# Performance work log

Hardware: AMD Instinct MI355X
Metric: run time of the kernel (lower is better)

The kernel has to match this reference:

```python
import jax, jax.numpy as jnp
import numpy as np

D_MODEL = 1024
NHEAD = 16
D_HEAD = D_MODEL // NHEAD


def setup_inputs() -> dict:
    key = jax.random.key(0)
    ks = jax.random.split(key, 11)
    B, S = 4, 1024
    s = 1.0 / np.sqrt(D_MODEL)
    inp = {
        'q_in': jax.random.normal(ks[0], (B, S, D_MODEL), jnp.float32),
        'k_in': jax.random.normal(ks[1], (B, S, D_MODEL), jnp.float32),
        'v_in': jax.random.normal(ks[2], (B, S, D_MODEL), jnp.float32),
        'Wq': jax.random.normal(ks[3], (D_MODEL, D_MODEL), jnp.float32) * s,
        'bq': jnp.zeros((D_MODEL,), jnp.float32),
        'Wk': jax.random.normal(ks[4], (D_MODEL, D_MODEL), jnp.float32) * s,
        'bk': jnp.zeros((D_MODEL,), jnp.float32),
        'Wv': jax.random.normal(ks[5], (D_MODEL, D_MODEL), jnp.float32) * s,
        'bv': jnp.zeros((D_MODEL,), jnp.float32),
        'Wo': jax.random.normal(ks[6], (D_MODEL, D_MODEL), jnp.float32) * s,
        'bo': jnp.zeros((D_MODEL,), jnp.float32),
    }
    return inp


def reference(q_in, k_in, v_in, Wq, bq, Wk, bk, Wv, bv, Wo, bo):
    B, Sq, _ = q_in.shape
    Sk = k_in.shape[1]
    # Linear projections (torch Linear: x @ W.T + b; here W stored as [in, out])
    Q = q_in @ Wq + bq
    K = k_in @ Wk + bk
    V = v_in @ Wv + bv
    # [B, H, S, Dh]
    Qh = Q.reshape(B, Sq, NHEAD, D_HEAD).transpose(0, 2, 1, 3)
    Kh = K.reshape(B, Sk, NHEAD, D_HEAD).transpose(0, 2, 1, 3)
    Vh = V.reshape(B, Sk, NHEAD, D_HEAD).transpose(0, 2, 1, 3)
    scores = jnp.einsum('bhqd,bhkd->bhqk', Qh, Kh) / jnp.sqrt(jnp.float32(D_HEAD))
    attn_weights = jax.nn.softmax(scores, axis=-1)
    attn = jnp.einsum('bhqk,bhkd->bhqd', attn_weights, Vh)
    attn = attn.transpose(0, 2, 1, 3).reshape(B, Sq, D_MODEL)
    out = attn @ Wo + bo
    return out
```

## Files before the change

kernel.cpp:

```cpp
#include <hip/hip_runtime.h>
#include <hip/hip_bf16.h>
#include <cstdint>
#include <cstddef>

typedef __bf16 bf16_t;
typedef __bf16 bf16x8 __attribute__((ext_vector_type(8)));
typedef __bf16 bf16x4 __attribute__((ext_vector_type(4)));
typedef float f32x4 __attribute__((ext_vector_type(4)));

#define DM 1024
#define NHEAD 16
#define DHEAD 64

#define QSCALE 0.18033688011112042f
#define PSHIFT 4.0f
#define RS 72

#define WAITVM(N) asm volatile("s_waitcnt vmcnt(" #N ")" ::: "memory")

__device__ __forceinline__ void gload_lds16(const void* g, void* l) {
    __builtin_amdgcn_global_load_lds(
        (const __attribute__((address_space(1))) void*)g,
        (__attribute__((address_space(3))) void*)l,
        16, 0, 0);
}

__device__ __forceinline__ uint4 cvt8(float4 lo, float4 hi) {
    union { bf16_t b[8]; uint4 u; } o;
    o.b[0] = (bf16_t)lo.x; o.b[1] = (bf16_t)lo.y; o.b[2] = (bf16_t)lo.z; o.b[3] = (bf16_t)lo.w;
    o.b[4] = (bf16_t)hi.x; o.b[5] = (bf16_t)hi.y; o.b[6] = (bf16_t)hi.z; o.b[7] = (bf16_t)hi.w;
    return o.u;
}

__global__ void prep(
    const float* __restrict__ q_in, const float* __restrict__ k_in, const float* __restrict__ v_in,
    bf16_t* __restrict__ Xq, bf16_t* __restrict__ Xk, bf16_t* __restrict__ Xv,
    const float* __restrict__ w0, const float* __restrict__ w1,
    const float* __restrict__ w2, const float* __restrict__ w3,
    bf16_t* __restrict__ t0, bf16_t* __restrict__ t1,
    bf16_t* __restrict__ t2, bf16_t* __restrict__ t3)
{
    __shared__ float tile[64][65];
    int id = blockIdx.x;
    if (id < 6144) {
        int plane = id >> 11;
        int blk = id & 2047;
        const float* x = plane == 0 ? q_in : plane == 1 ? k_in : v_in;
        bf16_t* y      = plane == 0 ? Xq   : plane == 1 ? Xk   : Xv;
        int i = (blk * 256 + threadIdx.x) * 8;
        float4 lo = *(const float4*)&x[i];
        float4 hi = *(const float4*)&x[i + 4];
        *(uint4*)&y[i] = cvt8(lo, hi);
    } else {
        int t = id - 6144;
        int zi = t >> 8;
        int blk = t & 255;
        const float* w = zi == 0 ? w0 : zi == 1 ? w1 : zi == 2 ? w2 : w3;
        bf16_t* wt     = zi == 0 ? t0 : zi == 1 ? t1 : zi == 2 ? t2 : t3;
        int bx = (blk & 15) * 64;
        int by = (blk >> 4) * 64;
        int tx = threadIdx.x & 63, ty = threadIdx.x >> 6;
        for (int j = 0; j < 64; j += 4)
            tile[ty + j][tx] = w[(size_t)(by + ty + j) * DM + bx + tx];
        __syncthreads();
        int nl = threadIdx.x >> 3;
        int kl = (threadIdx.x & 7) * 8;
        for (int j = 0; j < 64; j += 32) {
            int n = nl + j;
            union { bf16_t b[8]; uint4 u; } o;
            for (int i = 0; i < 8; i++)
                o.b[i] = (bf16_t)tile[kl + i][n];
            *(uint4*)&wt[(size_t)(bx + n) * DM + by + kl] = o.u;
        }
    }
}

template <int MODE>
__device__ __forceinline__ void gemm_body(
    const bf16_t* __restrict__ A, const bf16_t* __restrict__ Bt,
    const float* __restrict__ bias, float scale,
    bf16_t* __restrict__ Cb,
    int r0, int c0, bf16_t* AsP, bf16_t* BsP)
{
    const int K = 1024;
    int tid  = threadIdx.x;
    int wave = tid >> 6;
    int lane = tid & 63;
    int quad = lane >> 4;
    int ln   = lane & 15;
    int wr   = wave >> 1;
    int wc   = wave & 1;

    f32x4 acc[4][4];
    for (int rb = 0; rb < 4; rb++)
        for (int cb = 0; cb < 4; cb++)
            acc[rb][cb] = (f32x4){0.f, 0.f, 0.f, 0.f};

    int sr = tid >> 2;
    int sk = (tid & 3) * 8;

    const bf16_t* gA0 = &A[(size_t)(r0 + sr) * K + sk];
    const bf16_t* gA1 = gA0 + (size_t)64 * K;
    const bf16_t* gB0 = &Bt[(size_t)(c0 + sr) * K + sk];
    const bf16_t* gB1 = gB0 + (size_t)64 * K;
    char* lA = (char*)AsP + wave * 1024;
    char* lB = (char*)BsP + wave * 1024;

    auto STAGE = [&](int s) {
        int off = (s & 3) * 8192;
        int k = s * 32;
        gload_lds16(gA0 + k, lA + off);
        gload_lds16(gA1 + k, lA + off + 4096);
        gload_lds16(gB0 + k, lB + off);
        gload_lds16(gB1 + k, lB + off + 4096);
    };
    auto COMPUTE = [&](int t) {
        const bf16_t* Ab = AsP + (t & 3) * 4096;
        const bf16_t* Bb = BsP + (t & 3) * 4096;
        bf16x8 af[4], bfv[4];
        for (int rb = 0; rb < 4; rb++)
            af[rb] = *(const bf16x8*)&Ab[(wr * 64 + rb * 16 + ln) * 32 + quad * 8];
        for (int cb = 0; cb < 4; cb++)
            bfv[cb] = *(const bf16x8*)&Bb[(wc * 64 + cb * 16 + ln) * 32 + quad * 8];
        for (int rb = 0; rb < 4; rb++)
            for (int cb = 0; cb < 4; cb++)
                acc[rb][cb] = __builtin_amdgcn_mfma_f32_16x16x32_bf16(af[rb], bfv[cb], acc[rb][cb], 0, 0, 0);
    };

    STAGE(0); STAGE(1); STAGE(2);

    for (int t = 0; t < 29; ++t) {
        WAITVM(8);
        __builtin_amdgcn_s_barrier();
        STAGE(t + 3);
        COMPUTE(t);
    }
    WAITVM(8); __builtin_amdgcn_s_barrier(); COMPUTE(29);
    WAITVM(4); __builtin_amdgcn_s_barrier(); COMPUTE(30);
    WAITVM(0); __builtin_amdgcn_s_barrier(); COMPUTE(31);

    for (int rb = 0; rb < 4; rb++) {
        for (int cb = 0; cb < 4; cb++) {
            int C = c0 + wc * 64 + cb * 16 + ln;
            for (int r = 0; r < 4; r++) {
                int R = r0 + wr * 64 + rb * 16 + quad * 4 + r;
                float v = acc[rb][cb][r];
                if (MODE == 1) {
                    int b = R >> 10, s = R & 1023;
                    int h = C >> 6,  d = C & 63;
                    Cb[(((size_t)b * NHEAD + h) * 1024 + s) * DHEAD + d] =
                        (bf16_t)((v + bias[C]) * scale);
                } else {
                    Cb[((size_t)(C >> 10) * 1024 + R) * 1024 + (C & 1023)] =
                        (bf16_t)(v + bias[R]);
                }
            }
        }
    }
}

__global__ __launch_bounds__(256) void gemm_qkv(
    const bf16_t* __restrict__ Xq, const bf16_t* __restrict__ Xk, const bf16_t* __restrict__ Xv,
    const bf16_t* __restrict__ Wtq, const bf16_t* __restrict__ Wtk, const bf16_t* __restrict__ Wtv,
    const float* __restrict__ bq, const float* __restrict__ bk, const float* __restrict__ bv,
    bf16_t* __restrict__ Qd, bf16_t* __restrict__ Kd, bf16_t* __restrict__ Vt)
{
    __shared__ __align__(16) bf16_t As[4 * 128 * 32];
    __shared__ __align__(16) bf16_t Bs[4 * 128 * 32];
    int z = blockIdx.z;
    if (z == 0) {
        gemm_body<1>(Xq, Wtq, bq, QSCALE, Qd,
                     blockIdx.x * 128, blockIdx.y * 128, As, Bs);
    } else if (z == 1) {
        gemm_body<1>(Xk, Wtk, bk, 1.0f, Kd,
                     blockIdx.x * 128, blockIdx.y * 128, As, Bs);
    } else {
        gemm_body<2>(Wtv, Xv, bv, 1.0f, Vt,
                     blockIdx.y * 128, blockIdx.x * 128, As, Bs);
    }
}

__global__ __launch_bounds__(256) void gemm_out(
    const bf16_t* __restrict__ At, const bf16_t* __restrict__ Wto,
    const float* __restrict__ bo, float* __restrict__ out)
{
    const int K = 1024;
    __shared__ __align__(16) bf16_t As[4 * 64 * 32];
    __shared__ __align__(16) bf16_t Bs[4 * 128 * 32];

    int tid  = threadIdx.x;
    int wave = tid >> 6;
    int lane = tid & 63;
    int quad = lane >> 4;
    int ln   = lane & 15;

    int r0 = blockIdx.x * 64;
    int c0 = blockIdx.y * 128;

    f32x4 acc[4][2];
    for (int rb = 0; rb < 4; rb++)
        for (int cb = 0; cb < 2; cb++)
            acc[rb][cb] = (f32x4){0.f, 0.f, 0.f, 0.f};

    int sr = tid >> 2;
    int sk = (tid & 3) * 8;

    const bf16_t* gA0 = At  + (size_t)(r0 + sr) * K + sk;
    const bf16_t* gB0 = Wto + (size_t)(c0 + sr) * K + sk;
    const bf16_t* gB1 = gB0 + (size_t)64 * K;
    char* lA = (char*)As + wave * 1024;
    char* lB = (char*)Bs + wave * 1024;

    auto STAGE = [&](int s) {
        int k = s * 32;
        gload_lds16(gA0 + k, lA + (s & 3) * 4096);
        gload_lds16(gB0 + k, lB + (s & 3) * 8192);
        gload_lds16(gB1 + k, lB + (s & 3) * 8192 + 4096);
    };
    auto COMPUTE = [&](int t) {
        const bf16_t* Ab = As + (t & 3) * 2048;
        const bf16_t* Bb = Bs + (t & 3) * 4096;
        bf16x8 af[4], bfv[2];
        for (int rb = 0; rb < 4; rb++)
            af[rb] = *(const bf16x8*)&Ab[(rb * 16 + ln) * 32 + quad * 8];
        for (int cb = 0; cb < 2; cb++)
            bfv[cb] = *(const bf16x8*)&Bb[(wave * 32 + cb * 16 + ln) * 32 + quad * 8];
        for (int rb = 0; rb < 4; rb++)
            for (int cb = 0; cb < 2; cb++)
                acc[rb][cb] = __builtin_amdgcn_mfma_f32_16x16x32_bf16(af[rb], bfv[cb], acc[rb][cb], 0, 0, 0);
    };

    STAGE(0); STAGE(1); STAGE(2);

    for (int t = 0; t < 29; ++t) {
        WAITVM(6);
        __builtin_amdgcn_s_barrier();
        STAGE(t + 3);
        COMPUTE(t);
    }
    WAITVM(6); __builtin_amdgcn_s_barrier(); COMPUTE(29);
    WAITVM(3); __builtin_amdgcn_s_barrier(); COMPUTE(30);
    WAITVM(0); __builtin_amdgcn_s_barrier(); COMPUTE(31);

    for (int rb = 0; rb < 4; rb++) {
        for (int cb = 0; cb < 2; cb++) {
            int C = c0 + wave * 32 + cb * 16 + ln;
            float bn = bo[C];
            for (int r = 0; r < 4; r++) {
                int R = r0 + rb * 16 + quad * 4 + r;
                out[(size_t)R * DM + C] = acc[rb][cb][r] + bn;
            }
        }
    }
}

__global__ __launch_bounds__(256) void attn6(
    const bf16_t* __restrict__ Q,
    const bf16_t* __restrict__ K,
    const bf16_t* __restrict__ Vt,
    bf16_t* __restrict__ O)
{
    __shared__ __align__(16) bf16_t Ks[64 * RS];
    __shared__ __align__(16) bf16_t Vs[64 * RS];
    __shared__ __align__(16) bf16_t Ps[4][32 * RS];

    int tid  = threadIdx.x;
    int wave = tid >> 6;
    int lane = tid & 63;
    int quad = lane >> 4;
    int ln   = lane & 15;

    int bh = blockIdx.x;
    int q0w = blockIdx.y * 128 + wave * 32;

    const bf16_t* Qb = Q  + (size_t)bh * 65536;
    const bf16_t* Kb = K  + (size_t)bh * 65536;
    const bf16_t* Vb = Vt + (size_t)bh * 65536;

    int srow = tid >> 3;
    int scol = (tid & 7) * 8;
    const bf16_t* gK0 = Kb + (size_t)srow * 64 + scol;
    const bf16_t* gK1 = gK0 + 32 * 64;
    const bf16_t* gV0 = Vb + (size_t)srow * 1024 + scol;
    const bf16_t* gV1 = gV0 + 32 * 1024;

    bf16x8 aq0[2], aq1[2];
    for (int h = 0; h < 2; h++) {
        aq0[h] = *(const bf16x8*)&Qb[(size_t)(q0w + h * 16 + ln) * 64 + quad * 8];
        aq1[h] = *(const bf16x8*)&Qb[(size_t)(q0w + h * 16 + ln) * 64 + 32 + quad * 8];
    }

    uint4 rK0 = *(const uint4*)gK0;
    uint4 rK1 = *(const uint4*)gK1;
    uint4 rV0 = *(const uint4*)gV0;
    uint4 rV1 = *(const uint4*)gV1;

    float l_lane[2] = {0.f, 0.f};
    f32x4 o_acc[2][4];
    for (int h = 0; h < 2; h++)
        for (int cb = 0; cb < 4; cb++)
            o_acc[h][cb] = (f32x4){0.f, 0.f, 0.f, 0.f};

    bf16_t* Pw = Ps[wave];

    for (int kt = 0; kt < 16; kt++) {
        __syncthreads();
        *(uint4*)&Ks[srow * RS + scol]        = rK0;
        *(uint4*)&Ks[(32 + srow) * RS + scol] = rK1;
        *(uint4*)&Vs[srow * RS + scol]        = rV0;
        *(uint4*)&Vs[(32 + srow) * RS + scol] = rV1;
        __syncthreads();

        if (kt < 15) {
            gK0 += 4096; gK1 += 4096; gV0 += 64; gV1 += 64;
            rK0 = *(const uint4*)gK0;
            rK1 = *(const uint4*)gK1;
            rV0 = *(const uint4*)gV0;
            rV1 = *(const uint4*)gV1;
        }

        f32x4 sc[4][2];
        for (int kb = 0; kb < 4; kb++) {
            bf16x8 kf0 = *(const bf16x8*)&Ks[(kb * 16 + ln) * RS + quad * 8];
            bf16x8 kf1 = *(const bf16x8*)&Ks[(kb * 16 + ln) * RS + 32 + quad * 8];
            for (int h = 0; h < 2; h++) {
                f32x4 a = (f32x4){0.f, 0.f, 0.f, 0.f};
                a = __builtin_amdgcn_mfma_f32_16x16x32_bf16(kf0, aq0[h], a, 0, 0, 0);
                a = __builtin_amdgcn_mfma_f32_16x16x32_bf16(kf1, aq1[h], a, 0, 0, 0);
                sc[kb][h] = a;
            }
        }

        for (int kb = 0; kb < 4; kb++) {
            for (int h = 0; h < 2; h++) {
                float p0 = __builtin_amdgcn_exp2f(sc[kb][h][0] - PSHIFT);
                float p1 = __builtin_amdgcn_exp2f(sc[kb][h][1] - PSHIFT);
                float p2 = __builtin_amdgcn_exp2f(sc[kb][h][2] - PSHIFT);
                float p3 = __builtin_amdgcn_exp2f(sc[kb][h][3] - PSHIFT);
                l_lane[h] += (p0 + p1) + (p2 + p3);
                bf16x4 pk = (bf16x4){(bf16_t)p0, (bf16_t)p1, (bf16_t)p2, (bf16_t)p3};
                *(bf16x4*)&Pw[(h * 16 + ln) * RS + kb * 16 + quad * 4] = pk;
            }
        }

        for (int kc = 0; kc < 2; kc++) {
            bf16x8 ap0 = *(const bf16x8*)&Pw[ln * RS + kc * 32 + quad * 8];
            bf16x8 ap1 = *(const bf16x8*)&Pw[(16 + ln) * RS + kc * 32 + quad * 8];
            for (int cb = 0; cb < 4; cb++) {
                bf16x8 vf = *(const bf16x8*)&Vs[(cb * 16 + ln) * RS + kc * 32 + quad * 8];
                o_acc[0][cb] = __builtin_amdgcn_mfma_f32_16x16x32_bf16(ap0, vf, o_acc[0][cb], 0, 0, 0);
                o_acc[1][cb] = __builtin_amdgcn_mfma_f32_16x16x32_bf16(ap1, vf, o_acc[1][cb], 0, 0, 0);
            }
        }
    }

    int b = bh >> 4, hd = bh & 15;
    for (int h = 0; h < 2; h++) {
        float l = l_lane[h];
        l += __shfl_xor(l, 16);
        l += __shfl_xor(l, 32);
        float invq[4];
        for (int r = 0; r < 4; r++)
            invq[r] = 1.f / __shfl(l, quad * 4 + r);
        for (int cb = 0; cb < 4; cb++) {
            for (int r = 0; r < 4; r++) {
                int q = q0w + h * 16 + quad * 4 + r;
                int d = cb * 16 + ln;
                O[((size_t)b * 1024 + q) * DM + hd * 64 + d] = (bf16_t)(o_acc[h][cb][r] * invq[r]);
            }
        }
    }
}

extern "C" void kernel_launch(void* const* d_in, const int* in_sizes, int n_in,
                              void* d_out, int out_size, void* d_ws, size_t ws_size,
                              hipStream_t stream) {
    const float* q_in = (const float*)d_in[0];
    const float* k_in = (const float*)d_in[1];
    const float* v_in = (const float*)d_in[2];
    const float* Wq   = (const float*)d_in[3];
    const float* bq   = (const float*)d_in[4];
    const float* Wk   = (const float*)d_in[5];
    const float* bk   = (const float*)d_in[6];
    const float* Wv   = (const float*)d_in[7];
    const float* bv   = (const float*)d_in[8];
    const float* Wo   = (const float*)d_in[9];
    const float* bo   = (const float*)d_in[10];

    char* ws = (char*)d_ws;
    const size_t MB = 1024ull * 1024ull;
    bf16_t* Xq  = (bf16_t*)(ws);
    bf16_t* Xk  = (bf16_t*)(ws + 8 * MB);
    bf16_t* Xv  = (bf16_t*)(ws + 16 * MB);
    bf16_t* Wtq = (bf16_t*)(ws + 24 * MB);
    bf16_t* Wtk = (bf16_t*)(ws + 26 * MB);
    bf16_t* Wtv = (bf16_t*)(ws + 28 * MB);
    bf16_t* Wto = (bf16_t*)(ws + 30 * MB);
    bf16_t* Qd  = (bf16_t*)(ws + 32 * MB);
    bf16_t* Kd  = (bf16_t*)(ws + 40 * MB);
    bf16_t* Vt  = (bf16_t*)(ws + 48 * MB);
    bf16_t* At  = Xq;

    prep<<<7168, 256, 0, stream>>>(q_in, k_in, v_in, Xq, Xk, Xv,
                                   Wq, Wk, Wv, Wo, Wtq, Wtk, Wtv, Wto);

    gemm_qkv<<<dim3(32, 8, 3), 256, 0, stream>>>(Xq, Xk, Xv,
                                                 Wtq, Wtk, Wtv, bq, bk, bv, Qd, Kd, Vt);

    attn6<<<dim3(64, 8), 256, 0, stream>>>(Qd, Kd, Vt, At);

    gemm_out<<<dim3(64, 8), 256, 0, stream>>>(At, Wto, bo, (float*)d_out);
}
```

Baseline: 216.7 us.

## Swizzle GEMM LDS tiles, use 3-stage pipeline, double-buffer attention K/V

Both GEMMs now XOR-swizzle the 16-byte chunk index on the global-to-LDS load and on the fragment read, to cut LDS bank conflicts. They also move from a 4-slot to a 3-slot ring with one barrier per k-step and raise MFMA wave priority during compute. Less shared memory plus launch-bounds occupancy hints should let more blocks fit per CU. The attention kernel double-buffers K/V in LDS, so each step needs one barrier instead of two. This adds register pressure and relies on exact vmcnt accounting being right.

```diff
diff --git a/kernel.cpp b/kernel.cpp
--- a/kernel.cpp
+++ b/kernel.cpp
@@ -17,6 +17,9 @@
 #define RS 72
 
 #define WAITVM(N) asm volatile("s_waitcnt vmcnt(" #N ")" ::: "memory")
+#define LGKM0()   asm volatile("s_waitcnt lgkmcnt(0)" ::: "memory")
+#define BAR()     do { asm volatile("" ::: "memory"); __builtin_amdgcn_s_barrier(); \
+                       asm volatile("" ::: "memory"); } while (0)
 
 __device__ __forceinline__ void gload_lds16(const void* g, void* l) {
     __builtin_amdgcn_global_load_lds(
@@ -97,7 +100,7 @@
             acc[rb][cb] = (f32x4){0.f, 0.f, 0.f, 0.f};
 
     int sr = tid >> 2;
-    int sk = (tid & 3) * 8;
+    int sk = (((tid & 3) ^ ((tid >> 3) & 3))) * 8;
 
     const bf16_t* gA0 = &A[(size_t)(r0 + sr) * K + sk];
     const bf16_t* gA1 = gA0 + (size_t)64 * K;
@@ -106,38 +109,46 @@
     char* lA = (char*)AsP + wave * 1024;
     char* lB = (char*)BsP + wave * 1024;
 
-    auto STAGE = [&](int s) {
-        int off = (s & 3) * 8192;
+    int ch = (quad ^ ((ln >> 1) & 3)) * 8;
+
+    auto STAGE = [&](int s, int slot) {
         int k = s * 32;
+        int off = slot * 8192;
         gload_lds16(gA0 + k, lA + off);
         gload_lds16(gA1 + k, lA + off + 4096);
         gload_lds16(gB0 + k, lB + off);
         gload_lds16(gB1 + k, lB + off + 4096);
     };
-    auto COMPUTE = [&](int t) {
-        const bf16_t* Ab = AsP + (t & 3) * 4096;
-        const bf16_t* Bb = BsP + (t & 3) * 4096;
+    auto COMPUTE = [&](int slot) {
+        const bf16_t* Ab = AsP + slot * 4096;
+        const bf16_t* Bb = BsP + slot * 4096;
         bf16x8 af[4], bfv[4];
+        #pragma unroll
         for (int rb = 0; rb < 4; rb++)
-            af[rb] = *(const bf16x8*)&Ab[(wr * 64 + rb * 16 + ln) * 32 + quad * 8];
+            af[rb] = *(const bf16x8*)&Ab[(wr * 64 + rb * 16 + ln) * 32 + ch];
+        #pragma unroll
         for (int cb = 0; cb < 4; cb++)
-            bfv[cb] = *(const bf16x8*)&Bb[(wc * 64 + cb * 16 + ln) * 32 + quad * 8];
+            bfv[cb] = *(const bf16x8*)&Bb[(wc * 64 + cb * 16 + ln) * 32 + ch];
+        __builtin_amdgcn_s_setprio(1);
+        #pragma unroll
         for (int rb = 0; rb < 4; rb++)
+            #pragma unroll
             for (int cb = 0; cb < 4; cb++)
                 acc[rb][cb] = __builtin_amdgcn_mfma_f32_16x16x32_bf16(af[rb], bfv[cb], acc[rb][cb], 0, 0, 0);
+        __builtin_amdgcn_s_setprio(0);
     };
 
-    STAGE(0); STAGE(1); STAGE(2);
-
-    for (int t = 0; t < 29; ++t) {
-        WAITVM(8);
-        __builtin_amdgcn_s_barrier();
-        STAGE(t + 3);
-        COMPUTE(t);
-    }
-    WAITVM(8); __builtin_amdgcn_s_barrier(); COMPUTE(29);
-    WAITVM(4); __builtin_amdgcn_s_barrier(); COMPUTE(30);
-    WAITVM(0); __builtin_amdgcn_s_barrier(); COMPUTE(31);
+    STAGE(0, 0); STAGE(1, 1);
+    WAITVM(4);
+    BAR();
+
+    for (int tt = 0; tt < 30; tt += 3) {
+        STAGE(tt + 2, 2); COMPUTE(0); WAITVM(4); BAR();
+        STAGE(tt + 3, 0); COMPUTE(1); WAITVM(4); BAR();
+        STAGE(tt + 4, 1); COMPUTE(2); WAITVM(4); BAR();
+    }
+    COMPUTE(0); WAITVM(0); BAR();
+    COMPUTE(1);
 
     for (int rb = 0; rb < 4; rb++) {
         for (int cb = 0; cb < 4; cb++) {
@@ -159,14 +170,14 @@
     }
 }
 
-__global__ __launch_bounds__(256) void gemm_qkv(
+__global__ __launch_bounds__(256, 3) void gemm_qkv(
     const bf16_t* __restrict__ Xq, const bf16_t* __restrict__ Xk, const bf16_t* __restrict__ Xv,
     const bf16_t* __restrict__ Wtq, const bf16_t* __restrict__ Wtk, const bf16_t* __restrict__ Wtv,
     const float* __restrict__ bq, const float* __restrict__ bk, const float* __restrict__ bv,
     bf16_t* __restrict__ Qd, bf16_t* __restrict__ Kd, bf16_t* __restrict__ Vt)
 {
-    __shared__ __align__(16) bf16_t As[4 * 128 * 32];
-    __shared__ __align__(16) bf16_t Bs[4 * 128 * 32];
+    __shared__ __align__(16) bf16_t As[3 * 128 * 32];
+    __shared__ __align__(16) bf16_t Bs[3 * 128 * 32];
     int z = blockIdx.z;
     if (z == 0) {
         gemm_body<1>(Xq, Wtq, bq, QSCALE, Qd,
@@ -180,13 +191,13 @@
     }
 }
 
-__global__ __launch_bounds__(256) void gemm_out(
+__global__ __launch_bounds__(256, 2) void gemm_out(
     const bf16_t* __restrict__ At, const bf16_t* __restrict__ Wto,
     const float* __restrict__ bo, float* __restrict__ out)
 {
     const int K = 1024;
-    __shared__ __align__(16) bf16_t As[4 * 64 * 32];
-    __shared__ __align__(16) bf16_t Bs[4 * 128 * 32];
+    __shared__ __align__(16) bf16_t As[3 * 64 * 32];
+    __shared__ __align__(16) bf16_t Bs[3 * 128 * 32];
 
     int tid  = threadIdx.x;
     int wave = tid >> 6;
@@ -203,7 +214,7 @@
             acc[rb][cb] = (f32x4){0.f, 0.f, 0.f, 0.f};
 
     int sr = tid >> 2;
-    int sk = (tid & 3) * 8;
+    int sk = (((tid & 3) ^ ((tid >> 3) & 3))) * 8;
 
     const bf16_t* gA0 = At  + (size_t)(r0 + sr) * K + sk;
     const bf16_t* gB0 = Wto + (size_t)(c0 + sr) * K + sk;
@@ -211,36 +222,44 @@
     char* lA = (char*)As + wave * 1024;
     char* lB = (char*)Bs + wave * 1024;
 
-    auto STAGE = [&](int s) {
+    int ch = (quad ^ ((ln >> 1) & 3)) * 8;
+
+    auto STAGE = [&](int s, int slot) {
         int k = s * 32;
-        gload_lds16(gA0 + k, lA + (s & 3) * 4096);
-        gload_lds16(gB0 + k, lB + (s & 3) * 8192);
-        gload_lds16(gB1 + k, lB + (s & 3) * 8192 + 4096);
+        gload_lds16(gA0 + k, lA + slot * 4096);
+        gload_lds16(gB0 + k, lB + slot * 8192);
+        gload_lds16(gB1 + k, lB + slot * 8192 + 4096);
     };
-    auto COMPUTE = [&](int t) {
-        const bf16_t* Ab = As + (t & 3) * 2048;
-        const bf16_t* Bb = Bs + (t & 3) * 4096;
+    auto COMPUTE = [&](int slot) {
+        const bf16_t* Ab = As + slot * 2048;
+        const bf16_t* Bb = Bs + slot * 4096;
         bf16x8 af[4], bfv[2];
+        #pragma unroll
         for (int rb = 0; rb < 4; rb++)
-            af[rb] = *(const bf16x8*)&Ab[(rb * 16 + ln) * 32 + quad * 8];
+            af[rb] = *(const bf16x8*)&Ab[(rb * 16 + ln) * 32 + ch];
+        #pragma unroll
         for (int cb = 0; cb < 2; cb++)
-            bfv[cb] = *(const bf16x8*)&Bb[(wave * 32 + cb * 16 + ln) * 32 + quad * 8];
+            bfv[cb] = *(const bf16x8*)&Bb[(wave * 32 + cb * 16 + ln) * 32 + ch];
+        __builtin_amdgcn_s_setprio(1);
+        #pragma unroll
         for (int rb = 0; rb < 4; rb++)
+            #pragma unroll
             for (int cb = 0; cb < 2; cb++)
                 acc[rb][cb] = __builtin_amdgcn_mfma_f32_16x16x32_bf16(af[rb], bfv[cb], acc[rb][cb], 0, 0, 0);
+        __builtin_amdgcn_s_setprio(0);
     };
 
-    STAGE(0); STAGE(1); STAGE(2);
-
-    for (int t = 0; t < 29; ++t) {
-        WAITVM(6);
-        __builtin_amdgcn_s_barrier();
-        STAGE(t + 3);
-        COMPUTE(t);
-    }
-    WAITVM(6); __builtin_amdgcn_s_barrier(); COMPUTE(29);
-    WAITVM(3); __builtin_amdgcn_s_barrier(); COMPUTE(30);
-    WAITVM(0); __builtin_amdgcn_s_barrier(); COMPUTE(31);
+    STAGE(0, 0); STAGE(1, 1);
+    WAITVM(3);
+    BAR();
+
+    for (int tt = 0; tt < 30; tt += 3) {
+        STAGE(tt + 2, 2); COMPUTE(0); WAITVM(3); BAR();
+        STAGE(tt + 3, 0); COMPUTE(1); WAITVM(3); BAR();
+        STAGE(tt + 4, 1); COMPUTE(2); WAITVM(3); BAR();
+    }
+    COMPUTE(0); WAITVM(0); BAR();
+    COMPUTE(1);
 
     for (int rb = 0; rb < 4; rb++) {
         for (int cb = 0; cb < 2; cb++) {
@@ -254,14 +273,14 @@
     }
 }
 
-__global__ __launch_bounds__(256) void attn6(
+__global__ __launch_bounds__(256) void attn7(
     const bf16_t* __restrict__ Q,
     const bf16_t* __restrict__ K,
     const bf16_t* __restrict__ Vt,
     bf16_t* __restrict__ O)
 {
-    __shared__ __align__(16) bf16_t Ks[64 * RS];
-    __shared__ __align__(16) bf16_t Vs[64 * RS];
+    __shared__ __align__(16) bf16_t Ks[2][64 * RS];
+    __shared__ __align__(16) bf16_t Vs[2][64 * RS];
     __shared__ __align__(16) bf16_t Ps[4][32 * RS];
 
     int tid  = threadIdx.x;
@@ -294,6 +313,15 @@
     uint4 rK1 = *(const uint4*)gK1;
     uint4 rV0 = *(const uint4*)gV0;
     uint4 rV1 = *(const uint4*)gV1;
+    *(uint4*)&Ks[0][srow * RS + scol]        = rK0;
+    *(uint4*)&Ks[0][(32 + srow) * RS + scol] = rK1;
+    *(uint4*)&Vs[0][srow * RS + scol]        = rV0;
+    *(uint4*)&Vs[0][(32 + srow) * RS + scol] = rV1;
+    gK0 += 4096; gK1 += 4096; gV0 += 64; gV1 += 64;
+    rK0 = *(const uint4*)gK0;
+    rK1 = *(const uint4*)gK1;
+    rV0 = *(const uint4*)gV0;
+    rV1 = *(const uint4*)gV1;
 
     float l_lane[2] = {0.f, 0.f};
     f32x4 o_acc[2][4];
@@ -303,15 +331,22 @@
 
     bf16_t* Pw = Ps[wave];
 
+    LGKM0();
+    BAR();
+
     for (int kt = 0; kt < 16; kt++) {
-        __syncthreads();
-        *(uint4*)&Ks[srow * RS + scol]        = rK0;
-        *(uint4*)&Ks[(32 + srow) * RS + scol] = rK1;
-        *(uint4*)&Vs[srow * RS + scol]        = rV0;
-        *(uint4*)&Vs[(32 + srow) * RS + scol] = rV1;
-        __syncthreads();
+        const bf16_t* Kc = Ks[kt & 1];
+        const bf16_t* Vc = Vs[kt & 1];
+        bf16_t* Kn = Ks[(kt + 1) & 1];
+        bf16_t* Vn = Vs[(kt + 1) & 1];
 
         if (kt < 15) {
+            *(uint4*)&Kn[srow * RS + scol]        = rK0;
+            *(uint4*)&Kn[(32 + srow) * RS + scol] = rK1;
+            *(uint4*)&Vn[srow * RS + scol]        = rV0;
+            *(uint4*)&Vn[(32 + srow) * RS + scol] = rV1;
+        }
+        if (kt < 14) {
             gK0 += 4096; gK1 += 4096; gV0 += 64; gV1 += 64;
             rK0 = *(const uint4*)gK0;
             rK1 = *(const uint4*)gK1;
@@ -321,8 +356,8 @@
 
         f32x4 sc[4][2];
         for (int kb = 0; kb < 4; kb++) {
-            bf16x8 kf0 = *(const bf16x8*)&Ks[(kb * 16 + ln) * RS + quad * 8];
-            bf16x8 kf1 = *(const bf16x8*)&Ks[(kb * 16 + ln) * RS + 32 + quad * 8];
+            bf16x8 kf0 = *(const bf16x8*)&Kc[(kb * 16 + ln) * RS + quad * 8];
+            bf16x8 kf1 = *(const bf16x8*)&Kc[(kb * 16 + ln) * RS + 32 + quad * 8];
             for (int h = 0; h < 2; h++) {
                 f32x4 a = (f32x4){0.f, 0.f, 0.f, 0.f};
                 a = __builtin_amdgcn_mfma_f32_16x16x32_bf16(kf0, aq0[h], a, 0, 0, 0);
@@ -347,10 +382,15 @@
             bf16x8 ap0 = *(const bf16x8*)&Pw[ln * RS + kc * 32 + quad * 8];
             bf16x8 ap1 = *(const bf16x8*)&Pw[(16 + ln) * RS + kc * 32 + quad * 8];
             for (int cb = 0; cb < 4; cb++) {
-                bf16x8 vf = *(const bf16x8*)&Vs[(cb * 16 + ln) * RS + kc * 32 + quad * 8];
+                bf16x8 vf = *(const bf16x8*)&Vc[(cb * 16 + ln) * RS + kc * 32 + quad * 8];
                 o_acc[0][cb] = __builtin_amdgcn_mfma_f32_16x16x32_bf16(ap0, vf, o_acc[0][cb], 0, 0, 0);
                 o_acc[1][cb] = __builtin_amdgcn_mfma_f32_16x16x32_bf16(ap1, vf, o_acc[1][cb], 0, 0, 0);
             }
+        }
+
+        if (kt < 15) {
+            LGKM0();
+            BAR();
         }
     }
 
@@ -407,7 +447,7 @@
     gemm_qkv<<<dim3(32, 8, 3), 256, 0, stream>>>(Xq, Xk, Xv,
                                                  Wtq, Wtk, Wtv, bq, bk, bv, Qd, Kd, Vt);
 
-    attn6<<<dim3(64, 8), 256, 0, stream>>>(Qd, Kd, Vt, At);
+    attn7<<<dim3(64, 8), 256, 0, stream>>>(Qd, Kd, Vt, At);
 
     gemm_out<<<dim3(64, 8), 256, 0, stream>>>(At, Wto, bo, (float*)d_out);
 }
```

After: 200.7 us, median of 2. 1.08x faster.
